# Performance work log

Hardware: AMD Instinct MI355X
Metric: run time of the kernel (lower is better)

The kernel has to match this reference:

```python
import jax, jax.numpy as jnp
import numpy as np

B, S, H, D, OUT = 4, 2048, 16, 64, 1024


def setup_inputs() -> dict:
    root = jax.random.key(0)
    ks = jax.random.split(root, 7)
    scale = 0.02
    return {
        "query": jax.random.normal(ks[0], (B, S, D), dtype=jnp.float32),
        "key": jax.random.normal(ks[1], (B, S, D), dtype=jnp.float32),
        "value": jax.random.normal(ks[2], (B, S, D), dtype=jnp.float32),
        # per-head projection weights, torch Linear layout [out, in] stacked over heads
        "Wq": jax.random.normal(ks[3], (H, D, D), dtype=jnp.float32) * scale,
        "Wk": jax.random.normal(ks[4], (H, D, D), dtype=jnp.float32) * scale,
        "Wv": jax.random.normal(ks[5], (H, D, D), dtype=jnp.float32) * scale,
        # output projection weight [output_dim, H*D]
        "Wo": jax.random.normal(ks[6], (OUT, H * D), dtype=jnp.float32) * scale,
    }


def reference(query, key, value, Wq, Wk, Wv, Wo):
    b, s, d = query.shape
    h = Wq.shape[0]
    # per-head linear projections (x @ W_h.T), batched over all heads at once
    q = jnp.einsum('bsd,hed->bhse', query, Wq)   # [B,H,S,D]
    k = jnp.einsum('bsd,hed->bhse', key, Wk)
    v = jnp.einsum('bsd,hed->bhse', value, Wv)
    scores = jnp.einsum('bhqe,bhke->bhqk', q, k) / jnp.sqrt(jnp.asarray(d, q.dtype))
    attn = jax.nn.softmax(scores, axis=-1)       # [B,H,S,S]
    o = jnp.einsum('bhqk,bhke->bhqe', attn, v)   # [B,H,S,D]
    # concat heads along feature dim -> [B,S,H*D]
    x = o.transpose(0, 2, 1, 3).reshape(b, s, h * d)
    return x @ Wo.T                               # [B,S,OUT]
```

## Files before the change

kernel.cpp:

```cpp
#include <hip/hip_runtime.h>
#include <hip/hip_bf16.h>
#include <cstdint>


#define QSCALE 0.1803368801111204f

typedef __attribute__((ext_vector_type(8))) short bf16x8;
typedef __attribute__((ext_vector_type(4))) short bf16x4;
typedef __attribute__((ext_vector_type(2))) float f32x2;
typedef __attribute__((ext_vector_type(4))) float f32x4;
typedef __attribute__((ext_vector_type(16))) float f32x16;

typedef __attribute__((address_space(1))) unsigned int g_u32;
typedef __attribute__((address_space(3))) unsigned int l_u32;

__device__ inline unsigned cvt_pk_bf16(float a, float b) {
    unsigned r;
    asm("v_cvt_pk_bf16_f32 %0, %1, %2" : "=v"(r) : "v"(a), "v"(b));
    return r;
}

__device__ inline unsigned short f2bf1(float x) {
    return (unsigned short)cvt_pk_bf16(x, x);
}

__device__ inline uint2 pack4(float a, float b, float c, float d) {
    uint2 u; u.x = cvt_pk_bf16(a, b); u.y = cvt_pk_bf16(c, d); return u;
}

__device__ inline f32x4 mfma16(bf16x8 a, bf16x8 b, f32x4 c) {
    return __builtin_amdgcn_mfma_f32_16x16x32_bf16(a, b, c, 0, 0, 0);
}
__device__ inline f32x16 mfma32(bf16x8 a, bf16x8 b, f32x16 c) {
    return __builtin_amdgcn_mfma_f32_32x32x16_bf16(a, b, c, 0, 0, 0);
}

__device__ inline float sum16v(const f32x16& v) {
    const f32x2* p = reinterpret_cast<const f32x2*>(&v);
    f32x2 q0 = p[0] + p[1], q1 = p[2] + p[3], q2 = p[4] + p[5], q3 = p[6] + p[7];
    f32x2 r0 = q0 + q1, r1 = q2 + q3;
    f32x2 t = r0 + r1;
    return t[0] + t[1];
}

__global__ __launch_bounds__(256) void wo_conv(const float* __restrict__ Wo,
                                               unsigned short* __restrict__ Wob) {
    int i = (blockIdx.x * 256 + threadIdx.x) * 8;
    float4 f0 = *reinterpret_cast<const float4*>(Wo + i);
    float4 f1 = *reinterpret_cast<const float4*>(Wo + i + 4);
    uint4 h;
    h.x = cvt_pk_bf16(f0.x, f0.y); h.y = cvt_pk_bf16(f0.z, f0.w);
    h.z = cvt_pk_bf16(f1.x, f1.y); h.w = cvt_pk_bf16(f1.z, f1.w);
    *reinterpret_cast<uint4*>(Wob + i) = h;
}

__global__ __launch_bounds__(256) void qkv_proj(
    const float* __restrict__ q_in, const float* __restrict__ k_in,
    const float* __restrict__ v_in,
    const float* __restrict__ Wq, const float* __restrict__ Wk,
    const float* __restrict__ Wv,
    unsigned short* __restrict__ Qp, unsigned short* __restrict__ Kp,
    unsigned short* __restrict__ Vt) {
    const int z = blockIdx.z;
    const float* X = (z == 0) ? q_in : (z == 1) ? k_in : v_in;
    const float* W = (z == 0) ? Wq : (z == 1) ? Wk : Wv;
    const int bh = blockIdx.y;
    const int b = bh >> 4, h = bh & 15;
    const int s0 = blockIdx.x * 64;
    const int t = threadIdx.x;
    const int w = t >> 6, l = t & 63, lr = l & 15, lg = l >> 4;

    __shared__ unsigned short Xs[64][72];
    __shared__ unsigned short Ws[64][72];

    {
        const float* src = X + (size_t)(b * 2048 + s0) * 64;
        const float* wsrc = W + (size_t)h * 4096;
#pragma unroll
        for (int i = 0; i < 4; ++i) {
            int idx = t + i * 256;
            int r = idx >> 4, c4 = (idx & 15) * 4;
            float4 f = *reinterpret_cast<const float4*>(src + r * 64 + c4);
            *reinterpret_cast<uint2*>(&Xs[r][c4]) = pack4(f.x, f.y, f.z, f.w);
            float4 g = *reinterpret_cast<const float4*>(wsrc + r * 64 + c4);
            *reinterpret_cast<uint2*>(&Ws[r][c4]) = pack4(g.x, g.y, g.z, g.w);
        }
    }
    __syncthreads();

    f32x4 acc[4];
#pragma unroll
    for (int nt = 0; nt < 4; ++nt) acc[nt] = f32x4{0.f, 0.f, 0.f, 0.f};

    const size_t bhS = (size_t)bh * 2048 * 64;
    if (z < 2) {
#pragma unroll
        for (int kk = 0; kk < 2; ++kk) {
            bf16x8 a = *reinterpret_cast<const bf16x8*>(&Xs[w * 16 + lr][kk * 32 + lg * 8]);
#pragma unroll
            for (int nt = 0; nt < 4; ++nt) {
                bf16x8 bb = *reinterpret_cast<const bf16x8*>(&Ws[nt * 16 + lr][kk * 32 + lg * 8]);
                acc[nt] = mfma16(bb, a, acc[nt]);
            }
        }
        unsigned short* Out = (z == 0) ? Qp : Kp;
        const float scale = (z == 0) ? QSCALE : 1.0f;
        const int s = s0 + w * 16 + lr;
#pragma unroll
        for (int nt = 0; nt < 4; ++nt) {
            *reinterpret_cast<uint2*>(&Out[bhS + (size_t)s * 64 + nt * 16 + lg * 4]) =
                pack4(acc[nt][0] * scale, acc[nt][1] * scale,
                      acc[nt][2] * scale, acc[nt][3] * scale);
        }
    } else {
#pragma unroll
        for (int kk = 0; kk < 2; ++kk) {
            bf16x8 a = *reinterpret_cast<const bf16x8*>(&Xs[w * 16 + lr][kk * 32 + lg * 8]);
#pragma unroll
            for (int nt = 0; nt < 4; ++nt) {
                bf16x8 bb = *reinterpret_cast<const bf16x8*>(&Ws[nt * 16 + lr][kk * 32 + lg * 8]);
                acc[nt] = mfma16(a, bb, acc[nt]);
            }
        }
#pragma unroll
        for (int nt = 0; nt < 4; ++nt) {
            int e = nt * 16 + lr;
            int s = s0 + w * 16 + lg * 4;
            *reinterpret_cast<uint2*>(&Vt[(size_t)bh * 64 * 2048 + (size_t)e * 2048 + s]) =
                pack4(acc[nt][0], acc[nt][1], acc[nt][2], acc[nt][3]);
        }
    }
}

__global__ __launch_bounds__(256, 4) void attn_kernel(
    const unsigned short* __restrict__ Qp, const unsigned short* __restrict__ Kp,
    const unsigned short* __restrict__ Vt, unsigned short* __restrict__ Xb) {
    const int id = blockIdx.x + 16 * blockIdx.y;
    const int bh = id & 63;
    const int qx = id >> 6;
    const int b = bh >> 4, h = bh & 15;
    const int t = threadIdx.x;
    const int w = t >> 6, l = t & 63;
    const int lo = l & 31, hi = l >> 5;
    const int qw = qx * 128 + w * 32;

    __shared__ unsigned short Kbuf[2][4096];
    __shared__ unsigned short Vbuf[2][4096];

    bf16x8 bq[4];
    {
        const unsigned short* qptr = Qp + ((size_t)bh * 2048 + qw + lo) * 64 + hi * 8;
#pragma unroll
        for (int ds = 0; ds < 4; ++ds)
            bq[ds] = *reinterpret_cast<const bf16x8*>(qptr + ds * 16);
    }

    f32x16 oacc0, oacc1;
#pragma unroll
    for (int r = 0; r < 16; ++r) { oacc0[r] = 0.f; oacc1[r] = 0.f; }
    float lsum = 0.f;

    const unsigned short* kbase = Kp + (size_t)bh * 2048 * 64;
    const unsigned short* vbase = Vt + (size_t)bh * 64 * 2048;

    const int rr = l >> 3;
    const int sp = (l & 7) ^ rr;
    const int rb = w * 16;

#pragma unroll
    for (int i = 0; i < 2; ++i) {
        int r = rb + i * 8 + rr;
        __builtin_amdgcn_global_load_lds(
            (const g_u32*)(kbase + (size_t)r * 64 + sp * 8),
            (l_u32*)(&Kbuf[0][(rb + i * 8) * 64]), 16, 0, 0);
        __builtin_amdgcn_global_load_lds(
            (const g_u32*)(vbase + (size_t)r * 2048 + sp * 8),
            (l_u32*)(&Vbuf[0][(rb + i * 8) * 64]), 16, 0, 0);
    }
    __syncthreads();

    const int swz = (lo & 7) << 4;

    for (int kt = 0; kt < 32; ++kt) {
        const int cur = kt & 1;
        if (kt < 31) {
#pragma unroll
            for (int i = 0; i < 2; ++i) {
                int r = rb + i * 8 + rr;
                __builtin_amdgcn_global_load_lds(
                    (const g_u32*)(kbase + (size_t)((kt + 1) * 64 + r) * 64 + sp * 8),
                    (l_u32*)(&Kbuf[cur ^ 1][(rb + i * 8) * 64]), 16, 0, 0);
                __builtin_amdgcn_global_load_lds(
                    (const g_u32*)(vbase + (size_t)r * 2048 + (kt + 1) * 64 + sp * 8),
                    (l_u32*)(&Vbuf[cur ^ 1][(rb + i * 8) * 64]), 16, 0, 0);
            }
        }

        const char* kb = (const char*)Kbuf[cur];
        const char* vb = (const char*)Vbuf[cur];

#pragma unroll
        for (int half = 0; half < 2; ++half) {
            f32x16 s;
#pragma unroll
            for (int r = 0; r < 16; ++r) s[r] = 0.f;
            const char* krow = kb + (lo + 32 * half) * 128;
            __builtin_amdgcn_s_setprio(1);
#pragma unroll
            for (int ds = 0; ds < 4; ++ds) {
                bf16x8 ka = *reinterpret_cast<const bf16x8*>(krow + ((32 * ds + 16 * hi) ^ swz));
                s = mfma32(ka, bq[ds], s);
            }
            __builtin_amdgcn_s_setprio(0);

#pragma unroll
            for (int r = 0; r < 16; ++r) s[r] = __builtin_amdgcn_exp2f(s[r]);
            lsum += sum16v(s);

#pragma unroll
            for (int ks2 = 0; ks2 < 2; ++ks2) {
                const int bb = ks2 * 8;
                unsigned w0 = cvt_pk_bf16(s[bb + 0], s[bb + 1]);
                unsigned w1 = cvt_pk_bf16(s[bb + 2], s[bb + 3]);
                unsigned w2 = cvt_pk_bf16(s[bb + 4], s[bb + 5]);
                unsigned w3 = cvt_pk_bf16(s[bb + 6], s[bb + 7]);
                asm("v_permlane32_swap_b32 %0, %1" : "+v"(w0), "+v"(w2));
                asm("v_permlane32_swap_b32 %0, %1" : "+v"(w1), "+v"(w3));
                union { unsigned u[4]; bf16x8 v; } pa;
                pa.u[0] = w0; pa.u[1] = w1; pa.u[2] = w2; pa.u[3] = w3;
                int c = (32 * (half * 2 + ks2) + 16 * hi) ^ swz;
                bf16x8 v0 = *reinterpret_cast<const bf16x8*>(vb + lo * 128 + c);
                bf16x8 v1 = *reinterpret_cast<const bf16x8*>(vb + (lo + 32) * 128 + c);
                __builtin_amdgcn_s_setprio(1);
                oacc0 = mfma32(pa.v, v0, oacc0);
                oacc1 = mfma32(pa.v, v1, oacc1);
                __builtin_amdgcn_s_setprio(0);
            }
        }
        __syncthreads();
    }

    lsum += __shfl_xor(lsum, 32);
    const size_t rowbase = (size_t)b * 2048 * 1024 + (size_t)h * 64;
#pragma unroll
    for (int r = 0; r < 16; ++r) {
        int ql = (r & 3) + 8 * (r >> 2) + 4 * hi;
        float inv = 1.0f / __shfl(lsum, ql);
        unsigned short* dst = Xb + rowbase + (size_t)(qw + ql) * 1024;
        dst[lo] = f2bf1(oacc0[r] * inv);
        dst[lo + 32] = f2bf1(oacc1[r] * inv);
    }
}

__global__ __launch_bounds__(256) void out_gemm(
    const unsigned short* __restrict__ Xb, const unsigned short* __restrict__ Wob,
    float* __restrict__ out) {
    const int wg = blockIdx.x + 8 * blockIdx.y;
    const int xcd = wg & 7, k2 = wg >> 3;
    const int mb = (xcd * 8 + (k2 & 7)) * 128;
    const int nb = (k2 >> 3) * 128;
    const int t = threadIdx.x;
    const int w = t >> 6, l = t & 63, lr = l & 15, lg = l >> 4;
    const int wr = (w >> 1) * 64, wc = (w & 1) * 64;

    __shared__ unsigned short As[2][128 * 64];
    __shared__ unsigned short Bs[2][128 * 64];

    f32x4 acc[4][4];
#pragma unroll
    for (int mi = 0; mi < 4; ++mi)
#pragma unroll
        for (int ni = 0; ni < 4; ++ni) acc[mi][ni] = f32x4{0.f, 0.f, 0.f, 0.f};

    const int rr = l >> 3;
    const int sp = (l & 7) ^ rr;
    const int swz = (lr & 7) << 4;

#pragma unroll
    for (int i = 0; i < 4; ++i) {
        int r = w * 32 + i * 8 + rr;
        __builtin_amdgcn_global_load_lds(
            (const g_u32*)(Xb + (size_t)(mb + r) * 1024 + sp * 8),
            (l_u32*)(&As[0][(w * 32 + i * 8) * 64]), 16, 0, 0);
        __builtin_amdgcn_global_load_lds(
            (const g_u32*)(Wob + (size_t)(nb + r) * 1024 + sp * 8),
            (l_u32*)(&Bs[0][(w * 32 + i * 8) * 64]), 16, 0, 0);
    }
    __syncthreads();

    for (int kt = 0; kt < 16; ++kt) {
        const int cur = kt & 1;
        if (kt < 15) {
#pragma unroll
            for (int i = 0; i < 4; ++i) {
                int r = w * 32 + i * 8 + rr;
                __builtin_amdgcn_global_load_lds(
                    (const g_u32*)(Xb + (size_t)(mb + r) * 1024 + (kt + 1) * 64 + sp * 8),
                    (l_u32*)(&As[cur ^ 1][(w * 32 + i * 8) * 64]), 16, 0, 0);
                __builtin_amdgcn_global_load_lds(
                    (const g_u32*)(Wob + (size_t)(nb + r) * 1024 + (kt + 1) * 64 + sp * 8),
                    (l_u32*)(&Bs[cur ^ 1][(w * 32 + i * 8) * 64]), 16, 0, 0);
            }
        }

        const char* ab = (const char*)As[cur];
        const char* bbp = (const char*)Bs[cur];
#pragma unroll
        for (int kk = 0; kk < 2; ++kk) {
            const int cb = (kk * 64 + lg * 16) ^ swz;
            bf16x8 af[4], bf[4];
#pragma unroll
            for (int mi = 0; mi < 4; ++mi)
                af[mi] = *reinterpret_cast<const bf16x8*>(ab + (wr + mi * 16 + lr) * 128 + cb);
#pragma unroll
            for (int ni = 0; ni < 4; ++ni)
                bf[ni] = *reinterpret_cast<const bf16x8*>(bbp + (wc + ni * 16 + lr) * 128 + cb);
            __builtin_amdgcn_s_setprio(1);
#pragma unroll
            for (int mi = 0; mi < 4; ++mi)
#pragma unroll
                for (int ni = 0; ni < 4; ++ni)
                    acc[mi][ni] = mfma16(bf[ni], af[mi], acc[mi][ni]);
            __builtin_amdgcn_s_setprio(0);
        }
        __syncthreads();
    }

#pragma unroll
    for (int mi = 0; mi < 4; ++mi) {
        const size_t row = (size_t)(mb + wr + mi * 16 + lr);
#pragma unroll
        for (int ni = 0; ni < 4; ++ni) {
            float4 o;
            o.x = acc[mi][ni][0]; o.y = acc[mi][ni][1];
            o.z = acc[mi][ni][2]; o.w = acc[mi][ni][3];
            *reinterpret_cast<float4*>(&out[row * 1024 + nb + wc + ni * 16 + lg * 4]) = o;
        }
    }
}

extern "C" void kernel_launch(void* const* d_in, const int* in_sizes, int n_in,
                              void* d_out, int out_size, void* d_ws, size_t ws_size,
                              hipStream_t stream) {
    (void)in_sizes; (void)n_in; (void)out_size; (void)ws_size;
    const float* query = (const float*)d_in[0];
    const float* key   = (const float*)d_in[1];
    const float* value = (const float*)d_in[2];
    const float* Wq = (const float*)d_in[3];
    const float* Wk = (const float*)d_in[4];
    const float* Wv = (const float*)d_in[5];
    const float* Wo = (const float*)d_in[6];
    float* out = (float*)d_out;

    char* ws = (char*)d_ws;
    unsigned short* Qp  = (unsigned short*)(ws);
    unsigned short* Kp  = (unsigned short*)(ws + (size_t)16 * 1024 * 1024);
    unsigned short* Vt  = (unsigned short*)(ws + (size_t)32 * 1024 * 1024);
    unsigned short* Xb  = (unsigned short*)(ws + (size_t)48 * 1024 * 1024);
    unsigned short* Wob = (unsigned short*)(ws + (size_t)64 * 1024 * 1024);

    hipLaunchKernelGGL(wo_conv, dim3(512), dim3(256), 0, stream, Wo, Wob);
    hipLaunchKernelGGL(qkv_proj, dim3(32, 64, 3), dim3(256), 0, stream,
                       query, key, value, Wq, Wk, Wv, Qp, Kp, Vt);
    hipLaunchKernelGGL(attn_kernel, dim3(16, 64), dim3(256), 0, stream,
                       Qp, Kp, Vt, Xb);
    hipLaunchKernelGGL(out_gemm, dim3(8, 64), dim3(256), 0, stream,
                       Xb, Wob, out);
}
```

Before: 202.1 us.

## Reuse input tile across all heads in QKV projection and pre-convert weights

Restructures the QKV projection so each block loads a 128-row input tile once, keeps it in registers, and loops over all 16 heads. This avoids re-reading fp32 inputs per head. Q/K/V weights are converted to bf16 in the existing weight-conversion kernel and read directly from global memory. The grid shrinks to 192 blocks, which may underfill the GPU and serialize more work per block.

```diff
diff --git a/kernel.cpp b/kernel.cpp
--- a/kernel.cpp
+++ b/kernel.cpp
@@ -6,7 +6,6 @@
 #define QSCALE 0.1803368801111204f
 
 typedef __attribute__((ext_vector_type(8))) short bf16x8;
-typedef __attribute__((ext_vector_type(4))) short bf16x4;
 typedef __attribute__((ext_vector_type(2))) float f32x2;
 typedef __attribute__((ext_vector_type(4))) float f32x4;
 typedef __attribute__((ext_vector_type(16))) float f32x16;
@@ -43,91 +42,116 @@
     return t[0] + t[1];
 }
 
-__global__ __launch_bounds__(256) void wo_conv(const float* __restrict__ Wo,
-                                               unsigned short* __restrict__ Wob) {
+__global__ __launch_bounds__(256) void wconv(
+    const float* __restrict__ wo, const float* __restrict__ wq,
+    const float* __restrict__ wk, const float* __restrict__ wv,
+    unsigned short* __restrict__ wob, unsigned short* __restrict__ wqb,
+    unsigned short* __restrict__ wkb, unsigned short* __restrict__ wvb) {
+    const int y = blockIdx.y;
+    const float* src = (y == 0) ? wo : (y == 1) ? wq : (y == 2) ? wk : wv;
+    unsigned short* dst = (y == 0) ? wob : (y == 1) ? wqb : (y == 2) ? wkb : wvb;
+    const int n = (y == 0) ? 1048576 : 65536;
     int i = (blockIdx.x * 256 + threadIdx.x) * 8;
-    float4 f0 = *reinterpret_cast<const float4*>(Wo + i);
-    float4 f1 = *reinterpret_cast<const float4*>(Wo + i + 4);
+    if (i >= n) return;
+    float4 f0 = *reinterpret_cast<const float4*>(src + i);
+    float4 f1 = *reinterpret_cast<const float4*>(src + i + 4);
     uint4 h;
     h.x = cvt_pk_bf16(f0.x, f0.y); h.y = cvt_pk_bf16(f0.z, f0.w);
     h.z = cvt_pk_bf16(f1.x, f1.y); h.w = cvt_pk_bf16(f1.z, f1.w);
-    *reinterpret_cast<uint4*>(Wob + i) = h;
+    *reinterpret_cast<uint4*>(dst + i) = h;
 }
 
 __global__ __launch_bounds__(256) void qkv_proj(
     const float* __restrict__ q_in, const float* __restrict__ k_in,
     const float* __restrict__ v_in,
-    const float* __restrict__ Wq, const float* __restrict__ Wk,
-    const float* __restrict__ Wv,
+    const unsigned short* __restrict__ Wqb, const unsigned short* __restrict__ Wkb,
+    const unsigned short* __restrict__ Wvb,
     unsigned short* __restrict__ Qp, unsigned short* __restrict__ Kp,
     unsigned short* __restrict__ Vt) {
-    const int z = blockIdx.z;
+    const int z = blockIdx.y;
     const float* X = (z == 0) ? q_in : (z == 1) ? k_in : v_in;
-    const float* W = (z == 0) ? Wq : (z == 1) ? Wk : Wv;
-    const int bh = blockIdx.y;
-    const int b = bh >> 4, h = bh & 15;
-    const int s0 = blockIdx.x * 64;
+    const unsigned short* W = (z == 0) ? Wqb : (z == 1) ? Wkb : Wvb;
+    const int srow0 = blockIdx.x * 128;
+    const int b = srow0 >> 11;
+    const int sb = srow0 & 2047;
     const int t = threadIdx.x;
     const int w = t >> 6, l = t & 63, lr = l & 15, lg = l >> 4;
 
-    __shared__ unsigned short Xs[64][72];
-    __shared__ unsigned short Ws[64][72];
+    __shared__ unsigned short Xs[128][72];
 
     {
-        const float* src = X + (size_t)(b * 2048 + s0) * 64;
-        const float* wsrc = W + (size_t)h * 4096;
-#pragma unroll
-        for (int i = 0; i < 4; ++i) {
+        const float* src = X + (size_t)srow0 * 64;
+#pragma unroll
+        for (int i = 0; i < 8; ++i) {
             int idx = t + i * 256;
             int r = idx >> 4, c4 = (idx & 15) * 4;
             float4 f = *reinterpret_cast<const float4*>(src + r * 64 + c4);
             *reinterpret_cast<uint2*>(&Xs[r][c4]) = pack4(f.x, f.y, f.z, f.w);
-            float4 g = *reinterpret_cast<const float4*>(wsrc + r * 64 + c4);
-            *reinterpret_cast<uint2*>(&Ws[r][c4]) = pack4(g.x, g.y, g.z, g.w);
         }
     }
     __syncthreads();
 
-    f32x4 acc[4];
-#pragma unroll
-    for (int nt = 0; nt < 4; ++nt) acc[nt] = f32x4{0.f, 0.f, 0.f, 0.f};
-
-    const size_t bhS = (size_t)bh * 2048 * 64;
-    if (z < 2) {
-#pragma unroll
-        for (int kk = 0; kk < 2; ++kk) {
-            bf16x8 a = *reinterpret_cast<const bf16x8*>(&Xs[w * 16 + lr][kk * 32 + lg * 8]);
-#pragma unroll
-            for (int nt = 0; nt < 4; ++nt) {
-                bf16x8 bb = *reinterpret_cast<const bf16x8*>(&Ws[nt * 16 + lr][kk * 32 + lg * 8]);
-                acc[nt] = mfma16(bb, a, acc[nt]);
-            }
-        }
-        unsigned short* Out = (z == 0) ? Qp : Kp;
-        const float scale = (z == 0) ? QSCALE : 1.0f;
-        const int s = s0 + w * 16 + lr;
-#pragma unroll
-        for (int nt = 0; nt < 4; ++nt) {
-            *reinterpret_cast<uint2*>(&Out[bhS + (size_t)s * 64 + nt * 16 + lg * 4]) =
-                pack4(acc[nt][0] * scale, acc[nt][1] * scale,
-                      acc[nt][2] * scale, acc[nt][3] * scale);
-        }
-    } else {
-#pragma unroll
-        for (int kk = 0; kk < 2; ++kk) {
-            bf16x8 a = *reinterpret_cast<const bf16x8*>(&Xs[w * 16 + lr][kk * 32 + lg * 8]);
-#pragma unroll
-            for (int nt = 0; nt < 4; ++nt) {
-                bf16x8 bb = *reinterpret_cast<const bf16x8*>(&Ws[nt * 16 + lr][kk * 32 + lg * 8]);
-                acc[nt] = mfma16(a, bb, acc[nt]);
-            }
-        }
-#pragma unroll
-        for (int nt = 0; nt < 4; ++nt) {
-            int e = nt * 16 + lr;
-            int s = s0 + w * 16 + lg * 4;
-            *reinterpret_cast<uint2*>(&Vt[(size_t)bh * 64 * 2048 + (size_t)e * 2048 + s]) =
-                pack4(acc[nt][0], acc[nt][1], acc[nt][2], acc[nt][3]);
+    bf16x8 xf[2][2];
+#pragma unroll
+    for (int sf = 0; sf < 2; ++sf)
+#pragma unroll
+        for (int kk = 0; kk < 2; ++kk)
+            xf[sf][kk] = *reinterpret_cast<const bf16x8*>(&Xs[w * 32 + sf * 16 + lr][kk * 32 + lg * 8]);
+
+    for (int h = 0; h < 16; ++h) {
+        const unsigned short* Wh = W + h * 4096;
+        bf16x8 wf[4][2];
+#pragma unroll
+        for (int nt = 0; nt < 4; ++nt)
+#pragma unroll
+            for (int kk = 0; kk < 2; ++kk)
+                wf[nt][kk] = *reinterpret_cast<const bf16x8*>(Wh + (nt * 16 + lr) * 64 + kk * 32 + lg * 8);
+
+        const size_t bhS = (size_t)(b * 16 + h) * 2048 * 64;
+        f32x4 acc[4][2];
+#pragma unroll
+        for (int nt = 0; nt < 4; ++nt)
+#pragma unroll
+            for (int sf = 0; sf < 2; ++sf) acc[nt][sf] = f32x4{0.f, 0.f, 0.f, 0.f};
+
+        if (z < 2) {
+#pragma unroll
+            for (int kk = 0; kk < 2; ++kk)
+#pragma unroll
+                for (int nt = 0; nt < 4; ++nt)
+#pragma unroll
+                    for (int sf = 0; sf < 2; ++sf)
+                        acc[nt][sf] = mfma16(wf[nt][kk], xf[sf][kk], acc[nt][sf]);
+            unsigned short* Out = (z == 0) ? Qp : Kp;
+            const float scale = (z == 0) ? QSCALE : 1.0f;
+#pragma unroll
+            for (int nt = 0; nt < 4; ++nt)
+#pragma unroll
+                for (int sf = 0; sf < 2; ++sf) {
+                    int s = sb + w * 32 + sf * 16 + lr;
+                    int e0 = nt * 16 + lg * 4;
+                    *reinterpret_cast<uint2*>(&Out[bhS + (size_t)s * 64 + e0]) =
+                        pack4(acc[nt][sf][0] * scale, acc[nt][sf][1] * scale,
+                              acc[nt][sf][2] * scale, acc[nt][sf][3] * scale);
+                }
+        } else {
+#pragma unroll
+            for (int kk = 0; kk < 2; ++kk)
+#pragma unroll
+                for (int nt = 0; nt < 4; ++nt)
+#pragma unroll
+                    for (int sf = 0; sf < 2; ++sf)
+                        acc[nt][sf] = mfma16(xf[sf][kk], wf[nt][kk], acc[nt][sf]);
+#pragma unroll
+            for (int nt = 0; nt < 4; ++nt)
+#pragma unroll
+                for (int sf = 0; sf < 2; ++sf) {
+                    int e = nt * 16 + lr;
+                    int s4 = sb + w * 32 + sf * 16 + lg * 4;
+                    *reinterpret_cast<uint2*>(
+                        &Vt[(size_t)(b * 16 + h) * 64 * 2048 + (size_t)e * 2048 + s4]) =
+                        pack4(acc[nt][sf][0], acc[nt][sf][1], acc[nt][sf][2], acc[nt][sf][3]);
+                }
         }
     }
 }
@@ -358,10 +382,14 @@
     unsigned short* Vt  = (unsigned short*)(ws + (size_t)32 * 1024 * 1024);
     unsigned short* Xb  = (unsigned short*)(ws + (size_t)48 * 1024 * 1024);
     unsigned short* Wob = (unsigned short*)(ws + (size_t)64 * 1024 * 1024);
-
-    hipLaunchKernelGGL(wo_conv, dim3(512), dim3(256), 0, stream, Wo, Wob);
-    hipLaunchKernelGGL(qkv_proj, dim3(32, 64, 3), dim3(256), 0, stream,
-                       query, key, value, Wq, Wk, Wv, Qp, Kp, Vt);
+    unsigned short* Wqb = (unsigned short*)(ws + (size_t)66 * 1024 * 1024);
+    unsigned short* Wkb = Wqb + 65536;
+    unsigned short* Wvb = Wkb + 65536;
+
+    hipLaunchKernelGGL(wconv, dim3(512, 4), dim3(256), 0, stream,
+                       Wo, Wq, Wk, Wv, Wob, Wqb, Wkb, Wvb);
+    hipLaunchKernelGGL(qkv_proj, dim3(64, 3), dim3(256), 0, stream,
+                       query, key, value, Wqb, Wkb, Wvb, Qp, Kp, Vt);
     hipLaunchKernelGGL(attn_kernel, dim3(16, 64), dim3(256), 0, stream,
                        Qp, Kp, Vt, Xb);
     hipLaunchKernelGGL(out_gemm, dim3(8, 64), dim3(256), 0, stream,
```

Measured after the change: 207.4 us. +2.6%, slower.

## Restructure QKV projection as tiled GEMM and fold Wo conversion into it

Applied to the files above, without the earlier changes.

The per-(batch,head) 64x64 projection kernel is replaced by a single GEMM over all B*S rows times all H*D output columns, using 128x128 tiles with XOR-swizzled shared memory. This raises the reuse of each loaded input tile and cuts how often the fp32 inputs are re-read per head. The separate Wo bf16 conversion kernel is merged into the same launch as an extra z-slice, removing one kernel launch. In exchange the kernel uses more registers per thread and launches fewer, larger blocks.

```diff
diff --git a/kernel.cpp b/kernel.cpp
--- a/kernel.cpp
+++ b/kernel.cpp
@@ -6,7 +6,6 @@
 #define QSCALE 0.1803368801111204f
 
 typedef __attribute__((ext_vector_type(8))) short bf16x8;
-typedef __attribute__((ext_vector_type(4))) short bf16x4;
 typedef __attribute__((ext_vector_type(2))) float f32x2;
 typedef __attribute__((ext_vector_type(4))) float f32x4;
 typedef __attribute__((ext_vector_type(16))) float f32x16;
@@ -43,91 +42,123 @@
     return t[0] + t[1];
 }
 
-__global__ __launch_bounds__(256) void wo_conv(const float* __restrict__ Wo,
-                                               unsigned short* __restrict__ Wob) {
-    int i = (blockIdx.x * 256 + threadIdx.x) * 8;
-    float4 f0 = *reinterpret_cast<const float4*>(Wo + i);
-    float4 f1 = *reinterpret_cast<const float4*>(Wo + i + 4);
-    uint4 h;
-    h.x = cvt_pk_bf16(f0.x, f0.y); h.y = cvt_pk_bf16(f0.z, f0.w);
-    h.z = cvt_pk_bf16(f1.x, f1.y); h.w = cvt_pk_bf16(f1.z, f1.w);
-    *reinterpret_cast<uint4*>(Wob + i) = h;
-}
-
-__global__ __launch_bounds__(256) void qkv_proj(
+__global__ __launch_bounds__(256) void qkv_gemm(
     const float* __restrict__ q_in, const float* __restrict__ k_in,
     const float* __restrict__ v_in,
     const float* __restrict__ Wq, const float* __restrict__ Wk,
-    const float* __restrict__ Wv,
+    const float* __restrict__ Wv, const float* __restrict__ Wo,
     unsigned short* __restrict__ Qp, unsigned short* __restrict__ Kp,
-    unsigned short* __restrict__ Vt) {
+    unsigned short* __restrict__ Vt, unsigned short* __restrict__ Wob) {
     const int z = blockIdx.z;
+    const int t = threadIdx.x;
+
+    if (z == 3) {
+        int id = blockIdx.x + 64 * blockIdx.y;
+        int i = (id * 256 + t) * 8;
+        float4 f0 = *reinterpret_cast<const float4*>(Wo + i);
+        float4 f1 = *reinterpret_cast<const float4*>(Wo + i + 4);
+        uint4 h;
+        h.x = cvt_pk_bf16(f0.x, f0.y); h.y = cvt_pk_bf16(f0.z, f0.w);
+        h.z = cvt_pk_bf16(f1.x, f1.y); h.w = cvt_pk_bf16(f1.z, f1.w);
+        *reinterpret_cast<uint4*>(Wob + i) = h;
+        return;
+    }
+
     const float* X = (z == 0) ? q_in : (z == 1) ? k_in : v_in;
     const float* W = (z == 0) ? Wq : (z == 1) ? Wk : Wv;
-    const int bh = blockIdx.y;
-    const int b = bh >> 4, h = bh & 15;
-    const int s0 = blockIdx.x * 64;
-    const int t = threadIdx.x;
+    const int mb = blockIdx.x * 128;
+    const int nb = blockIdx.y * 128;
     const int w = t >> 6, l = t & 63, lr = l & 15, lg = l >> 4;
-
-    __shared__ unsigned short Xs[64][72];
-    __shared__ unsigned short Ws[64][72];
-
-    {
-        const float* src = X + (size_t)(b * 2048 + s0) * 64;
-        const float* wsrc = W + (size_t)h * 4096;
-#pragma unroll
-        for (int i = 0; i < 4; ++i) {
-            int idx = t + i * 256;
-            int r = idx >> 4, c4 = (idx & 15) * 4;
-            float4 f = *reinterpret_cast<const float4*>(src + r * 64 + c4);
-            *reinterpret_cast<uint2*>(&Xs[r][c4]) = pack4(f.x, f.y, f.z, f.w);
-            float4 g = *reinterpret_cast<const float4*>(wsrc + r * 64 + c4);
-            *reinterpret_cast<uint2*>(&Ws[r][c4]) = pack4(g.x, g.y, g.z, g.w);
-        }
+    const int wr = (w >> 1) * 64, wc = (w & 1) * 64;
+
+    __shared__ char XsB[16384];
+    __shared__ char WsB[16384];
+
+#pragma unroll
+    for (int i = 0; i < 4; ++i) {
+        int idx = t + i * 256;
+        int r = idx >> 3, sg = idx & 7;
+        const float* xp = X + (size_t)(mb + r) * 64 + sg * 8;
+        float4 f0 = *reinterpret_cast<const float4*>(xp);
+        float4 f1 = *reinterpret_cast<const float4*>(xp + 4);
+        uint4 hx;
+        hx.x = cvt_pk_bf16(f0.x, f0.y); hx.y = cvt_pk_bf16(f0.z, f0.w);
+        hx.z = cvt_pk_bf16(f1.x, f1.y); hx.w = cvt_pk_bf16(f1.z, f1.w);
+        *reinterpret_cast<uint4*>(XsB + ((r * 128 + sg * 16) ^ ((r & 7) << 4))) = hx;
+        const float* wp = W + (size_t)(nb + r) * 64 + sg * 8;
+        float4 g0 = *reinterpret_cast<const float4*>(wp);
+        float4 g1 = *reinterpret_cast<const float4*>(wp + 4);
+        uint4 hw;
+        hw.x = cvt_pk_bf16(g0.x, g0.y); hw.y = cvt_pk_bf16(g0.z, g0.w);
+        hw.z = cvt_pk_bf16(g1.x, g1.y); hw.w = cvt_pk_bf16(g1.z, g1.w);
+        *reinterpret_cast<uint4*>(WsB + ((r * 128 + sg * 16) ^ ((r & 7) << 4))) = hw;
     }
     __syncthreads();
 
-    f32x4 acc[4];
-#pragma unroll
-    for (int nt = 0; nt < 4; ++nt) acc[nt] = f32x4{0.f, 0.f, 0.f, 0.f};
-
-    const size_t bhS = (size_t)bh * 2048 * 64;
+    f32x4 acc[4][4];
+#pragma unroll
+    for (int mi = 0; mi < 4; ++mi)
+#pragma unroll
+        for (int ni = 0; ni < 4; ++ni) acc[mi][ni] = f32x4{0.f, 0.f, 0.f, 0.f};
+
+    const int sx = (lr & 7) << 4;
+#pragma unroll
+    for (int kk = 0; kk < 2; ++kk) {
+        const int cb = kk * 64 + lg * 16;
+        bf16x8 af[4], bf[4];
+#pragma unroll
+        for (int mi = 0; mi < 4; ++mi)
+            af[mi] = *reinterpret_cast<const bf16x8*>(
+                XsB + (((wr + mi * 16 + lr) * 128 + cb) ^ sx));
+#pragma unroll
+        for (int ni = 0; ni < 4; ++ni)
+            bf[ni] = *reinterpret_cast<const bf16x8*>(
+                WsB + (((wc + ni * 16 + lr) * 128 + cb) ^ sx));
+        if (z < 2) {
+#pragma unroll
+            for (int mi = 0; mi < 4; ++mi)
+#pragma unroll
+                for (int ni = 0; ni < 4; ++ni)
+                    acc[mi][ni] = mfma16(bf[ni], af[mi], acc[mi][ni]);
+        } else {
+#pragma unroll
+            for (int mi = 0; mi < 4; ++mi)
+#pragma unroll
+                for (int ni = 0; ni < 4; ++ni)
+                    acc[mi][ni] = mfma16(af[mi], bf[ni], acc[mi][ni]);
+        }
+    }
+
+    const int h = (nb + wc) >> 6;
     if (z < 2) {
-#pragma unroll
-        for (int kk = 0; kk < 2; ++kk) {
-            bf16x8 a = *reinterpret_cast<const bf16x8*>(&Xs[w * 16 + lr][kk * 32 + lg * 8]);
-#pragma unroll
-            for (int nt = 0; nt < 4; ++nt) {
-                bf16x8 bb = *reinterpret_cast<const bf16x8*>(&Ws[nt * 16 + lr][kk * 32 + lg * 8]);
-                acc[nt] = mfma16(bb, a, acc[nt]);
-            }
-        }
         unsigned short* Out = (z == 0) ? Qp : Kp;
-        const float scale = (z == 0) ? QSCALE : 1.0f;
-        const int s = s0 + w * 16 + lr;
-#pragma unroll
-        for (int nt = 0; nt < 4; ++nt) {
-            *reinterpret_cast<uint2*>(&Out[bhS + (size_t)s * 64 + nt * 16 + lg * 4]) =
-                pack4(acc[nt][0] * scale, acc[nt][1] * scale,
-                      acc[nt][2] * scale, acc[nt][3] * scale);
+        const float sc = (z == 0) ? QSCALE : 1.0f;
+#pragma unroll
+        for (int mi = 0; mi < 4; ++mi) {
+            int srow = mb + wr + mi * 16 + lr;
+            int b = srow >> 11, s = srow & 2047;
+            size_t base = (size_t)(b * 16 + h) * 131072 + (size_t)s * 64;
+#pragma unroll
+            for (int ni = 0; ni < 4; ++ni) {
+                int e = ni * 16 + lg * 4;
+                *reinterpret_cast<uint2*>(&Out[base + e]) =
+                    pack4(acc[mi][ni][0] * sc, acc[mi][ni][1] * sc,
+                          acc[mi][ni][2] * sc, acc[mi][ni][3] * sc);
+            }
         }
     } else {
 #pragma unroll
-        for (int kk = 0; kk < 2; ++kk) {
-            bf16x8 a = *reinterpret_cast<const bf16x8*>(&Xs[w * 16 + lr][kk * 32 + lg * 8]);
-#pragma unroll
-            for (int nt = 0; nt < 4; ++nt) {
-                bf16x8 bb = *reinterpret_cast<const bf16x8*>(&Ws[nt * 16 + lr][kk * 32 + lg * 8]);
-                acc[nt] = mfma16(a, bb, acc[nt]);
-            }
-        }
-#pragma unroll
-        for (int nt = 0; nt < 4; ++nt) {
-            int e = nt * 16 + lr;
-            int s = s0 + w * 16 + lg * 4;
-            *reinterpret_cast<uint2*>(&Vt[(size_t)bh * 64 * 2048 + (size_t)e * 2048 + s]) =
-                pack4(acc[nt][0], acc[nt][1], acc[nt][2], acc[nt][3]);
+        for (int mi = 0; mi < 4; ++mi) {
+            int srow = mb + wr + mi * 16 + lg * 4;
+            int b = srow >> 11, s = srow & 2047;
+            size_t base = (size_t)(b * 16 + h) * 131072;
+#pragma unroll
+            for (int ni = 0; ni < 4; ++ni) {
+                int e = ni * 16 + lr;
+                *reinterpret_cast<uint2*>(&Vt[base + (size_t)e * 2048 + s]) =
+                    pack4(acc[mi][ni][0], acc[mi][ni][1],
+                          acc[mi][ni][2], acc[mi][ni][3]);
+            }
         }
     }
 }
@@ -359,9 +390,8 @@
     unsigned short* Xb  = (unsigned short*)(ws + (size_t)48 * 1024 * 1024);
     unsigned short* Wob = (unsigned short*)(ws + (size_t)64 * 1024 * 1024);
 
-    hipLaunchKernelGGL(wo_conv, dim3(512), dim3(256), 0, stream, Wo, Wob);
-    hipLaunchKernelGGL(qkv_proj, dim3(32, 64, 3), dim3(256), 0, stream,
-                       query, key, value, Wq, Wk, Wv, Qp, Kp, Vt);
+    hipLaunchKernelGGL(qkv_gemm, dim3(64, 8, 4), dim3(256), 0, stream,
+                       query, key, value, Wq, Wk, Wv, Wo, Qp, Kp, Vt, Wob);
     hipLaunchKernelGGL(attn_kernel, dim3(16, 64), dim3(256), 0, stream,
                        Qp, Kp, Vt, Xb);
     hipLaunchKernelGGL(out_gemm, dim3(8, 64), dim3(256), 0, stream,
```

New measurement: 199.5 us. About the same (-1.3%).
